# Kernel tuning notes

Measured on AMD Instinct MI355X. Metric: run time of the kernel, lower is better.

The kernel has to match this reference:

```python
import jax, jax.numpy as jnp
import numpy as np

RARITY_ALPHA = 0.5


def _forward(obs_emb, observed_mask, lengths, avg_interval, var_prior_emb_tensor,
             rarity_W, adjI, p2s_W1, p2s_b1, p2s_W2, p2s_b2,
             Wu, bu, Wr, br, Wc, bc):
    B, T, N, D = obs_emb.shape
    I = jnp.eye(N, dtype=obs_emb.dtype)
    # hypernetwork conditioning vector per node (prior_to_state MLP); identical
    # across batch since var_prior_emb_tensor is repeated over the batch dim.
    vv = jax.nn.relu(var_prior_emb_tensor @ p2s_W1 + p2s_b1) @ p2s_W2 + p2s_b2  # [N,E]
    vv = jnp.broadcast_to(vv[None], (B, N, vv.shape[-1]))                        # [B,N,E]
    tot = observed_mask.sum(axis=1)  # var_total_obs [B,N]

    def gate(z, W, b):
        # MLP_Param: per-node weights W_n = sum_e vv[n,e]*W[e]; fused einsum avoids
        # materializing [B,N,2D+1,D].
        return jnp.einsum('bni,bne,eio->bno', z, vv, W) + jnp.einsum('bne,eo->bno', vv, b)

    def step_fn(carry, xs):
        h, out = carry
        cur_obs, m, cur_avg, step = xs  # [B,N,D], [B,N], [B,N], scalar
        rs = RARITY_ALPHA * jnp.tanh(cur_avg / (tot + 1.0))                  # [B,N]
        rmat = -rarity_W * jnp.abs(rs[:, :, None] - rs[:, None, :])          # [B,N,N]
        # adj_mask[b,i,j] = observed(b,i)*observed(b,j)  (column-set then row-zero)
        adj_mask = m[:, :, None] * m[:, None, :]
        cur_adj = adjI * (1.0 + rmat) * adj_mask * (1.0 - I) + I             # [B,N,N]
        x = jnp.concatenate([cur_obs, rs[..., None]], axis=-1)              # [B,N,D+1]
        comb = jnp.einsum('bij,bjf->bif', cur_adj,
                          jnp.concatenate([x, h], axis=-1))                  # [B,N,2D+1]
        r = jax.nn.sigmoid(gate(comb, Wr, br))
        u = jax.nn.sigmoid(gate(comb, Wu, bu))
        mm = m[..., None] > 0
        h1 = jnp.where(mm, r * h, h)                      # h[nodes_ind] = r*h[nodes_ind]
        cand = jnp.tanh(gate(jnp.concatenate([x, h1], axis=-1), Wc, bc))
        h2 = jnp.where(mm, (1.0 - u) * h1 + u * cand, h1)  # scatter back at observed nodes
        out = jnp.where((step == lengths - 1)[:, None, None], h2, out)
        return (h2, out), None

    h0 = jnp.zeros((B, N, D), obs_emb.dtype)
    xs = (obs_emb.transpose(1, 0, 2, 3), observed_mask.transpose(1, 0, 2),
          avg_interval.transpose(1, 0, 2), jnp.arange(T))
    (_, out), _ = jax.lax.scan(step_fn, (h0, jnp.zeros_like(h0)), xs)
    return out


def setup_inputs() -> dict:
    B, T, N, D, E = 32, 64, 128, 64, 5
    key = jax.random.key(0)
    ks = jax.random.split(key, 18)
    inp = {}
    inp['obs_emb'] = jax.random.normal(ks[0], (B, T, N, D), jnp.float32)
    inp['adj'] = jax.random.normal(ks[1], (N, N), jnp.float32)  # unused by forward
    inp['observed_mask'] = (jax.random.uniform(ks[2], (B, T, N)) < 0.5).astype(jnp.float32)
    inp['observed_tp'] = jax.random.uniform(ks[3], (B, T), jnp.float32)       # unused
    inp['tp_emb_tensor'] = jax.random.normal(ks[4], (B, T, 1), jnp.float32)   # unused
    inp['lengths'] = jax.random.randint(ks[5], (B,), T // 2, T + 1, jnp.int32)
    inp['avg_interval'] = jax.random.uniform(ks[6], (B, T, N), jnp.float32)
    inp['var_prior_emb_tensor'] = jax.random.normal(ks[7], (N, 768), jnp.float32)
    # learned parameters
    inp['rarity_W'] = jax.random.normal(ks[8], (N, N), jnp.float32)
    inp['adjI'] = jnp.eye(N, dtype=jnp.float32) + 0.01 * jax.random.normal(ks[9], (N, N), jnp.float32)
    inp['p2s_W1'] = 0.05 * jax.random.normal(ks[10], (768, 2 * D), jnp.float32)
    inp['p2s_b1'] = jnp.zeros((2 * D,), jnp.float32)
    inp['p2s_W2'] = 0.1 * jax.random.normal(ks[11], (2 * D, E), jnp.float32)
    inp['p2s_b2'] = jnp.zeros((E,), jnp.float32)
    inp['Wu'] = 0.1 * jax.random.normal(ks[12], (E, 2 * D + 1, D), jnp.float32)
    inp['bu'] = 0.1 * jax.random.normal(ks[13], (E, D), jnp.float32)
    inp['Wr'] = 0.1 * jax.random.normal(ks[14], (E, 2 * D + 1, D), jnp.float32)
    inp['br'] = 0.1 * jax.random.normal(ks[15], (E, D), jnp.float32)
    inp['Wc'] = 0.1 * jax.random.normal(ks[16], (E, 2 * D + 1, D), jnp.float32)
    inp['bc'] = 0.1 * jax.random.normal(ks[17], (E, D), jnp.float32)
    return inp


def reference(obs_emb, adj, observed_mask, observed_tp, tp_emb_tensor, lengths,
              avg_interval, var_prior_emb_tensor, rarity_W, adjI, p2s_W1, p2s_b1,
              p2s_W2, p2s_b2, Wu, bu, Wr, br, Wc, bc):
    # adj, observed_tp, tp_emb_tensor are accepted but never used, as in the torch code
    return _forward(obs_emb, observed_mask, lengths, avg_interval, var_prior_emb_tensor,
                    rarity_W, adjI, p2s_W1, p2s_b1, p2s_W2, p2s_b2,
                    Wu, bu, Wr, br, Wc, bc)
```

## Files before the change

### kernel.cpp

```cpp
#include <hip/hip_runtime.h>
#include <math.h>

constexpr size_t WS_VV  = 1024;
constexpr size_t WS_TOT = 2048;
constexpr size_t WS_RS  = 8192;
constexpr size_t WS_WH  = 270336;
constexpr size_t WS_WX  = 1843200;
constexpr size_t WS_BF  = 3440640;
constexpr size_t WS_H   = 3465216;
constexpr size_t WS_CH  = 3727360;
constexpr size_t WS_CX  = 3989504;
constexpr size_t WS_GXR = 8249344;
constexpr size_t WS_GXU = 12443648;
constexpr size_t WS_CXC = 16637952;

__device__ __forceinline__ float sigm(float x){ return 1.f/(1.f+expf(-x)); }

__device__ __forceinline__ float2 ld2_mall(const float* p){
  union { unsigned long long u; float2 f; } cv;
  cv.u = __hip_atomic_load((const unsigned long long*)p, __ATOMIC_RELAXED,
                           __HIP_MEMORY_SCOPE_AGENT);
  return cv.f;
}
__device__ __forceinline__ void st2_mall(float* p, float a, float b){
  union { unsigned long long u; float2 f; } cv;
  cv.f = make_float2(a, b);
  __hip_atomic_store((unsigned long long*)p, cv.u, __ATOMIC_RELAXED,
                     __HIP_MEMORY_SCOPE_AGENT);
}

__global__ void k_vv(const float* __restrict__ vpe, const float* __restrict__ W1,
                     const float* __restrict__ b1, const float* __restrict__ W2,
                     const float* __restrict__ b2, float* __restrict__ ws){
  int n = blockIdx.x, tid = threadIdx.x;
  __shared__ float hid[128];
  if (tid < 128){
    float acc = b1[tid];
    for (int k=0;k<768;k++) acc = fmaf(vpe[n*768+k], W1[k*128+tid], acc);
    hid[tid] = fmaxf(acc, 0.f);
  }
  __syncthreads();
  if (tid < 5){
    float acc = b2[tid];
    for (int h=0;h<128;h++) acc = fmaf(hid[h], W2[h*5+tid], acc);
    ws[WS_VV + n*5 + tid] = acc;
  }
}

__global__ void k_fold(const float* __restrict__ Wr, const float* __restrict__ Wu,
                       const float* __restrict__ Wc, const float* __restrict__ br,
                       const float* __restrict__ bu, const float* __restrict__ bc,
                       float* __restrict__ ws){
  int bid = blockIdx.x; int g = bid>>7; int n = bid&127;
  const float* W  = (g==0)?Wr:(g==1)?Wu:Wc;
  const float* bb = (g==0)?br:(g==1)?bu:bc;
  float v[5];
#pragma unroll
  for (int e=0;e<5;e++) v[e] = ws[WS_VV + n*5 + e];
  for (int idx=threadIdx.x; idx<129*64; idx+=256){
    int i = idx>>6, o = idx&63;
    float a = 0.f;
#pragma unroll
    for (int e=0;e<5;e++) a = fmaf(v[e], W[(e*129+i)*64+o], a);
    if (i < 65) ws[WS_WX + (size_t)(g*128+n)*4160 + i*64 + o] = a;
    else        ws[WS_WH + (size_t)(g*128+n)*4096 + (i-65)*64 + o] = a;
  }
  if (threadIdx.x < 64){
    int o = threadIdx.x; float a = 0.f;
#pragma unroll
    for (int e=0;e<5;e++) a = fmaf(v[e], bb[e*64+o], a);
    ws[WS_BF + (g*128+n)*64 + o] = a;
  }
}

__global__ void k_tot(const float* __restrict__ mask, float* __restrict__ ws){
  int id = blockIdx.x*256 + threadIdx.x;
  int b = id>>7, n = id&127;
  float s = 0.f;
  for (int t=0;t<64;t++) s += mask[(b*64+t)*128 + n];
  ws[WS_TOT + b*128 + n] = s;
}

__global__ void k_rs(const float* __restrict__ avg, float* __restrict__ ws){
  int id = blockIdx.x*256 + threadIdx.x;
  int b = id>>13, n = id&127;
  float tot = ws[WS_TOT + b*128 + n];
  ws[WS_RS + id] = 0.5f * tanhf(avg[id] / (tot + 1.f));
}

__global__ __launch_bounds__(256) void p4a(const float* __restrict__ obs,
      const float* __restrict__ mask, const float* __restrict__ adjI,
      const float* __restrict__ rW, const int* __restrict__ lengths,
      float* __restrict__ ws, int c0){
  int rc = blockIdx.x;
  int b = rc>>4, tl = rc&15, t = c0 + tl;
  if (t >= lengths[b]) return;
  int rt = b*64 + t;
  __shared__ float xt[64*68];
  __shared__ float adjh[128*68];
  __shared__ float rs_l[128], m_l[128];
  int tid = threadIdx.x;
  if (tid < 128){ rs_l[tid] = ws[WS_RS + rt*128 + tid]; m_l[tid] = mask[rt*128 + tid]; }
  __syncthreads();
  int it = tid>>3, ft = tid&7, i0 = it*4, f0 = ft*8;
  float4 aL[4], aH[4]; float a64[4];
#pragma unroll
  for (int ii=0;ii<4;ii++){ aL[ii]=make_float4(0,0,0,0); aH[ii]=make_float4(0,0,0,0); a64[ii]=0.f; }
  for (int half=0; half<2; half++){
    __syncthreads();
    int j0 = half*64;
    for (int idx=tid; idx<4096; idx+=256){
      int jl = idx>>6, f = idx&63;
      xt[jl*68+f] = obs[(size_t)rt*8192 + (j0+jl)*64 + f];
    }
    if (tid < 64) xt[tid*68+64] = rs_l[j0+tid];
    for (int idx=tid; idx<8192; idx+=256){
      int i = idx>>6, jl = idx&63, j = j0+jl;
      float a;
      if (i == j) a = 1.f;
      else {
        int gi = i*128 + j;
        float dd = fabsf(rs_l[i] - rs_l[j]);
        a = adjI[gi] * (1.f - rW[gi]*dd) * m_l[i] * m_l[j];
      }
      adjh[i*68+jl] = a;
    }
    __syncthreads();
    for (int jb=0; jb<16; jb++){
      float4 av[4];
#pragma unroll
      for (int ii=0;ii<4;ii++) av[ii] = *(const float4*)&adjh[(i0+ii)*68 + jb*4];
#pragma unroll
      for (int jj=0;jj<4;jj++){
        int jl = jb*4 + jj;
        float4 xlo = *(const float4*)&xt[jl*68 + f0];
        float4 xhi = *(const float4*)&xt[jl*68 + f0 + 4];
        float xr = xt[jl*68 + 64];
#pragma unroll
        for (int ii=0;ii<4;ii++){
          float a = (jj==0)?av[ii].x:(jj==1)?av[ii].y:(jj==2)?av[ii].z:av[ii].w;
          aL[ii].x = fmaf(a, xlo.x, aL[ii].x); aL[ii].y = fmaf(a, xlo.y, aL[ii].y);
          aL[ii].z = fmaf(a, xlo.z, aL[ii].z); aL[ii].w = fmaf(a, xlo.w, aL[ii].w);
          aH[ii].x = fmaf(a, xhi.x, aH[ii].x); aH[ii].y = fmaf(a, xhi.y, aH[ii].y);
          aH[ii].z = fmaf(a, xhi.z, aH[ii].z); aH[ii].w = fmaf(a, xhi.w, aH[ii].w);
          a64[ii] = fmaf(a, xr, a64[ii]);
        }
      }
    }
  }
#pragma unroll
  for (int ii=0;ii<4;ii++){
    int i = i0 + ii;
    size_t base = WS_CX + (size_t)i*33280 + (size_t)rc*65 + f0;
    ws[base+0]=aL[ii].x; ws[base+1]=aL[ii].y; ws[base+2]=aL[ii].z; ws[base+3]=aL[ii].w;
    ws[base+4]=aH[ii].x; ws[base+5]=aH[ii].y; ws[base+6]=aH[ii].z; ws[base+7]=aH[ii].w;
    if (ft == 0) ws[WS_CX + (size_t)i*33280 + (size_t)rc*65 + 64] = a64[ii];
  }
}

__global__ __launch_bounds__(256) void p4b(const float* __restrict__ obs,
      const int* __restrict__ lengths, float* __restrict__ ws, int c0){
  int bid = blockIdx.x;
  int g = bid >> 9; int r2 = bid & 511; int n = r2 >> 2; int tile = r2 & 3;
  __shared__ float A[128*69];
  __shared__ float Wl[65*64];
  __shared__ float bl[64];
  __shared__ int slen[32];
  int tid = threadIdx.x;
  if (tid < 32) slen[tid] = lengths[tid];
  for (int idx=tid; idx<4160; idx+=256) Wl[idx] = ws[WS_WX + (size_t)(g*128+n)*4160 + idx];
  if (tid < 64) bl[tid] = ws[WS_BF + (g*128+n)*64 + tid];
  if (g < 2){
    const float* src = &ws[WS_CX + (size_t)n*33280 + (size_t)tile*8320];
    for (int idx=tid; idx<8320; idx+=256){
      int r = idx/65, f = idx - r*65;
      A[r*69+f] = src[idx];
    }
  } else {
    for (int idx=tid; idx<8320; idx+=256){
      int r = idx/65, f = idx - r*65;
      int grow = tile*128 + r;
      int gb = grow>>4, t = c0 + (grow&15);
      float v = (f < 64) ? obs[(size_t)(gb*64+t)*8192 + n*64 + f]
                         : ws[WS_RS + (gb*64+t)*128 + n];
      A[r*69+f] = v;
    }
  }
  __syncthreads();
  int rt8 = tid>>4, dq = tid&15;
  float4 acc[8];
#pragma unroll
  for (int rr=0;rr<8;rr++) acc[rr] = make_float4(0,0,0,0);
  for (int k=0;k<65;k++){
    float4 w = *(const float4*)&Wl[k*64 + dq*4];
#pragma unroll
    for (int rr=0;rr<8;rr++){
      float a = A[(rt8*8+rr)*69 + k];
      acc[rr].x = fmaf(a,w.x,acc[rr].x); acc[rr].y = fmaf(a,w.y,acc[rr].y);
      acc[rr].z = fmaf(a,w.z,acc[rr].z); acc[rr].w = fmaf(a,w.w,acc[rr].w);
    }
  }
  float4 b4 = *(const float4*)&bl[dq*4];
  float* dst = &ws[(g==0)?WS_GXR:(g==1)?WS_GXU:WS_CXC];
#pragma unroll
  for (int rr=0;rr<8;rr++){
    int grow = tile*128 + rt8*8 + rr;
    int gb = grow>>4, gtl = grow&15;
    if (c0 + gtl < slen[gb]){
      float4 o; o.x=acc[rr].x+b4.x; o.y=acc[rr].y+b4.y; o.z=acc[rr].z+b4.z; o.w=acc[rr].w+b4.w;
      *(float4*)&dst[((size_t)(n*16+gtl)*32 + gb)*64 + dq*4] = o;
    }
  }
}

__global__ __launch_bounds__(256) void krec(const float* __restrict__ mask,
      const int* __restrict__ lengths, const float* __restrict__ adjI,
      const float* __restrict__ rWm, float* __restrict__ out, float* __restrict__ ws,
      int c0){
  unsigned* hfl = (unsigned*)ws;
  const int bid = blockIdx.x, tid = threadIdx.x;
  const int bA = bid>>3, s = bid&7, ns = s*16;
  __shared__ float hs[8192];
  __shared__ float adjT[2560];
  __shared__ float chT[1088];
  __shared__ float hT[1088];
  __shared__ float rs_l[128], m_l[128];
  const int lenA = lengths[bA];
  const int ng = tid>>6, fA = tid&63;
  const int nl = tid>>4, fq = tid&15;
  const int n  = ns + nl;
  float* hbuf = &ws[WS_H];
  const float* wrg = &ws[WS_WH + (size_t)(0*128+n)*4096];
  const float* wug = &ws[WS_WH + (size_t)(1*128+n)*4096];
  const float* wcg = &ws[WS_WH + (size_t)(2*128+n)*4096];

  for (int t=c0; t<c0+16; t++){
    if (t >= lenA){
      if (tid == 0)
        __hip_atomic_store(&hfl[bid], (unsigned)(t+1), __ATOMIC_RELAXED,
                           __HIP_MEMORY_SCOPE_AGENT);
      __syncthreads();
      continue;
    }
    if (tid < 128) rs_l[tid] = ws[WS_RS + (size_t)(bA*64+t)*128 + tid];
    else           m_l[tid-128] = mask[(size_t)(bA*64+t)*128 + (tid-128)];
    __syncthreads();
    for (int idx=tid; idx<2048; idx+=256){
      int j = idx&127, il = idx>>7, I = ns+il;
      float a;
      if (I == j) a = 1.f;
      else {
        int gi = I*128 + j;
        float dd = fabsf(rs_l[I] - rs_l[j]);
        a = adjI[gi]*(1.f - rWm[gi]*dd)*m_l[I]*m_l[j];
      }
      adjT[j*20 + il] = a;
    }
    const int tl = t - c0;
    size_t gof = ((size_t)(n*16+tl)*32 + bA)*64 + fq*4;
    float4 arv = *(const float4*)&ws[WS_GXR + gof];
    float4 auv = *(const float4*)&ws[WS_GXU + gof];
    float4 acv = *(const float4*)&ws[WS_CXC + gof];
    float  msv = m_l[n];
    if (t > 0){
      if (tid < 8){
        unsigned tgt = (unsigned)t; int guard = 0;
        while (__hip_atomic_load(&hfl[bA*8 + tid], __ATOMIC_RELAXED,
                 __HIP_MEMORY_SCOPE_AGENT) < tgt && ++guard < (1<<20))
          __builtin_amdgcn_s_sleep(2);
      }
    }
    __syncthreads();
#pragma unroll
    for (int k=0;k<16;k++){
      int p = tid + 256*k;
      float2 v = ld2_mall(&hbuf[(size_t)bA*8192 + 2*p]);
      *(float2*)&hs[2*p] = v;
    }
    __syncthreads();
    float acc[4] = {0.f,0.f,0.f,0.f};
#pragma unroll 4
    for (int j=0;j<128;j++){
      float hv = hs[j*64 + fA];
      float4 a4 = *(const float4*)&adjT[j*20 + ng*4];
      acc[0] = fmaf(a4.x, hv, acc[0]);
      acc[1] = fmaf(a4.y, hv, acc[1]);
      acc[2] = fmaf(a4.z, hv, acc[2]);
      acc[3] = fmaf(a4.w, hv, acc[3]);
    }
#pragma unroll
    for (int r=0;r<4;r++) chT[(ng*4+r)*68 + fA] = acc[r];
    __syncthreads();
#pragma unroll 4
    for (int k=0;k<64;k++){
      float cv = chT[nl*68 + k];
      float4 wr4 = *(const float4*)&wrg[k*64 + fq*4];
      float4 wu4 = *(const float4*)&wug[k*64 + fq*4];
      arv.x = fmaf(cv,wr4.x,arv.x); arv.y = fmaf(cv,wr4.y,arv.y);
      arv.z = fmaf(cv,wr4.z,arv.z); arv.w = fmaf(cv,wr4.w,arv.w);
      auv.x = fmaf(cv,wu4.x,auv.x); auv.y = fmaf(cv,wu4.y,auv.y);
      auv.z = fmaf(cv,wu4.z,auv.z); auv.w = fmaf(cv,wu4.w,auv.w);
    }
    float4 rr4, uu4, h1;
    rr4.x = sigm(arv.x); rr4.y = sigm(arv.y); rr4.z = sigm(arv.z); rr4.w = sigm(arv.w);
    uu4.x = sigm(auv.x); uu4.y = sigm(auv.y); uu4.z = sigm(auv.z); uu4.w = sigm(auv.w);
    float4 hown = *(const float4*)&hs[n*64 + fq*4];
    bool ob = msv > 0.f;
    h1.x = ob ? rr4.x*hown.x : hown.x;
    h1.y = ob ? rr4.y*hown.y : hown.y;
    h1.z = ob ? rr4.z*hown.z : hown.z;
    h1.w = ob ? rr4.w*hown.w : hown.w;
    *(float4*)&hT[nl*68 + fq*4] = h1;
    __syncthreads();
#pragma unroll 4
    for (int k=0;k<64;k++){
      float hv1 = hT[nl*68 + k];
      float4 wc4 = *(const float4*)&wcg[k*64 + fq*4];
      acv.x = fmaf(hv1,wc4.x,acv.x); acv.y = fmaf(hv1,wc4.y,acv.y);
      acv.z = fmaf(hv1,wc4.z,acv.z); acv.w = fmaf(hv1,wc4.w,acv.w);
    }
    float4 cd, h2;
    cd.x = tanhf(acv.x); cd.y = tanhf(acv.y); cd.z = tanhf(acv.z); cd.w = tanhf(acv.w);
    h2.x = ob ? (1.f-uu4.x)*h1.x + uu4.x*cd.x : h1.x;
    h2.y = ob ? (1.f-uu4.y)*h1.y + uu4.y*cd.y : h1.y;
    h2.z = ob ? (1.f-uu4.z)*h1.z + uu4.z*cd.z : h1.z;
    h2.w = ob ? (1.f-uu4.w)*h1.w + uu4.w*cd.w : h1.w;
    float* hp = &hbuf[((size_t)bA*128 + n)*64 + fq*4];
    st2_mall(hp,   h2.x, h2.y);
    st2_mall(hp+2, h2.z, h2.w);
    if (t == lenA-1)
      *(float4*)&out[((size_t)bA*128 + n)*64 + fq*4] = h2;
    __syncthreads();
    asm volatile("s_waitcnt vmcnt(0)" ::: "memory");
    if (tid == 0)
      __hip_atomic_store(&hfl[bid], (unsigned)(t+1), __ATOMIC_RELAXED,
                         __HIP_MEMORY_SCOPE_AGENT);
  }
}

extern "C" void kernel_launch(void* const* d_in, const int* in_sizes, int n_in,
                              void* d_out, int out_size, void* d_ws, size_t ws_size,
                              hipStream_t stream){
  const float* obs  = (const float*)d_in[0];
  const float* maskp= (const float*)d_in[2];
  const int*   lens = (const int*)d_in[5];
  const float* avg  = (const float*)d_in[6];
  const float* vpe  = (const float*)d_in[7];
  const float* rW   = (const float*)d_in[8];
  const float* adjI = (const float*)d_in[9];
  const float* W1   = (const float*)d_in[10];
  const float* b1   = (const float*)d_in[11];
  const float* W2   = (const float*)d_in[12];
  const float* b2   = (const float*)d_in[13];
  const float* Wu   = (const float*)d_in[14];
  const float* bu   = (const float*)d_in[15];
  const float* Wr   = (const float*)d_in[16];
  const float* br   = (const float*)d_in[17];
  const float* Wc   = (const float*)d_in[18];
  const float* bc   = (const float*)d_in[19];
  float* out = (float*)d_out;
  float* ws  = (float*)d_ws;
  hipMemsetAsync(d_ws, 0, 4096, stream);
  hipMemsetAsync((char*)d_ws + WS_H*sizeof(float), 0, 262144*sizeof(float), stream);
  k_vv  <<<128, 256, 0, stream>>>(vpe, W1, b1, W2, b2, ws);
  k_fold<<<384, 256, 0, stream>>>(Wr, Wu, Wc, br, bu, bc, ws);
  k_tot <<<16,  256, 0, stream>>>(maskp, ws);
  k_rs  <<<1024,256, 0, stream>>>(avg, ws);
  for (int c = 0; c < 4; c++){
    int c0 = c*16;
    p4a <<<512, 256, 0, stream>>>(obs, maskp, adjI, rW, lens, ws, c0);
    p4b <<<1536,256, 0, stream>>>(obs, lens, ws, c0);
    krec<<<256, 256, 0, stream>>>(maskp, lens, adjI, rW, out, ws, c0);
  }
}
```

Before: 1.537 ms.

## Overlap recurrence with next-chunk projections in a fused double-buffered kernel

Time chunks shrink from 16 to 8 steps, and the adjacency-aggregation and input-projection workspaces become double-buffered. A single fused kernel per chunk runs the sequential recurrence blocks for chunk c alongside the aggregation (p4a) for chunk c+2 and the gate projections (p4b) for chunk c+1. Recurrence blocks get raised wave priority. The aim is to fill idle CUs during the latency-bound recurrence, which relies on cross-block spin-wait flags. The cost is twice as many launches and competition for memory bandwidth between the recurrence and the projection work.

```diff
diff --git a/kernel.cpp b/kernel.cpp
--- a/kernel.cpp
+++ b/kernel.cpp
@@ -8,11 +8,12 @@
 constexpr size_t WS_WX  = 1843200;
 constexpr size_t WS_BF  = 3440640;
 constexpr size_t WS_H   = 3465216;
-constexpr size_t WS_CH  = 3727360;
-constexpr size_t WS_CX  = 3989504;
-constexpr size_t WS_GXR = 8249344;
-constexpr size_t WS_GXU = 12443648;
-constexpr size_t WS_CXC = 16637952;
+constexpr size_t CXSZ   = 2129920;
+constexpr size_t GXSZ   = 2097152;
+constexpr size_t WS_CX0 = 3727360;
+constexpr size_t WS_GXR0= 7987200;
+constexpr size_t WS_GXU0= 12181504;
+constexpr size_t WS_CXC0= 16375808;
 
 __device__ __forceinline__ float sigm(float x){ return 1.f/(1.f+expf(-x)); }
 
@@ -88,17 +89,17 @@
   ws[WS_RS + id] = 0.5f * tanhf(avg[id] / (tot + 1.f));
 }
 
-__global__ __launch_bounds__(256) void p4a(const float* __restrict__ obs,
+__device__ void p4a_body(float* smem, const float* __restrict__ obs,
       const float* __restrict__ mask, const float* __restrict__ adjI,
       const float* __restrict__ rW, const int* __restrict__ lengths,
-      float* __restrict__ ws, int c0){
-  int rc = blockIdx.x;
-  int b = rc>>4, tl = rc&15, t = c0 + tl;
+      float* __restrict__ ws, int cc, int rc){
+  int b = rc>>3, tl = rc&7, t = cc*8 + tl;
   if (t >= lengths[b]) return;
   int rt = b*64 + t;
-  __shared__ float xt[64*68];
-  __shared__ float adjh[128*68];
-  __shared__ float rs_l[128], m_l[128];
+  float* xt   = smem;
+  float* adjh = smem + 4352;
+  float* rs_l = smem + 13056;
+  float* m_l  = smem + 13184;
   int tid = threadIdx.x;
   if (tid < 128){ rs_l[tid] = ws[WS_RS + rt*128 + tid]; m_l[tid] = mask[rt*128 + tid]; }
   __syncthreads();
@@ -148,30 +149,31 @@
       }
     }
   }
+  size_t cxb = WS_CX0 + (size_t)(cc&1)*CXSZ;
 #pragma unroll
   for (int ii=0;ii<4;ii++){
     int i = i0 + ii;
-    size_t base = WS_CX + (size_t)i*33280 + (size_t)rc*65 + f0;
+    size_t base = cxb + (size_t)i*16640 + (size_t)rc*65 + f0;
     ws[base+0]=aL[ii].x; ws[base+1]=aL[ii].y; ws[base+2]=aL[ii].z; ws[base+3]=aL[ii].w;
     ws[base+4]=aH[ii].x; ws[base+5]=aH[ii].y; ws[base+6]=aH[ii].z; ws[base+7]=aH[ii].w;
-    if (ft == 0) ws[WS_CX + (size_t)i*33280 + (size_t)rc*65 + 64] = a64[ii];
-  }
-}
-
-__global__ __launch_bounds__(256) void p4b(const float* __restrict__ obs,
-      const int* __restrict__ lengths, float* __restrict__ ws, int c0){
-  int bid = blockIdx.x;
-  int g = bid >> 9; int r2 = bid & 511; int n = r2 >> 2; int tile = r2 & 3;
-  __shared__ float A[128*69];
-  __shared__ float Wl[65*64];
-  __shared__ float bl[64];
-  __shared__ int slen[32];
+    if (ft == 0) ws[cxb + (size_t)i*16640 + (size_t)rc*65 + 64] = a64[ii];
+  }
+}
+
+__device__ void p4b_body(float* smem, const float* __restrict__ obs,
+      const int* __restrict__ lengths, float* __restrict__ ws, int cc, int pbid){
+  int g = pbid >> 8; int r2 = pbid & 255; int n = r2 >> 1; int tile = r2 & 1;
+  float* A  = smem;
+  float* Wl = smem + 8832;
+  float* bl = smem + 12992;
+  int* slen = (int*)(smem + 13056);
   int tid = threadIdx.x;
   if (tid < 32) slen[tid] = lengths[tid];
   for (int idx=tid; idx<4160; idx+=256) Wl[idx] = ws[WS_WX + (size_t)(g*128+n)*4160 + idx];
   if (tid < 64) bl[tid] = ws[WS_BF + (g*128+n)*64 + tid];
+  size_t cxb = WS_CX0 + (size_t)(cc&1)*CXSZ;
   if (g < 2){
-    const float* src = &ws[WS_CX + (size_t)n*33280 + (size_t)tile*8320];
+    const float* src = &ws[cxb + (size_t)n*16640 + (size_t)tile*8320];
     for (int idx=tid; idx<8320; idx+=256){
       int r = idx/65, f = idx - r*65;
       A[r*69+f] = src[idx];
@@ -180,7 +182,7 @@
     for (int idx=tid; idx<8320; idx+=256){
       int r = idx/65, f = idx - r*65;
       int grow = tile*128 + r;
-      int gb = grow>>4, t = c0 + (grow&15);
+      int gb = grow>>3, t = cc*8 + (grow&7);
       float v = (f < 64) ? obs[(size_t)(gb*64+t)*8192 + n*64 + f]
                          : ws[WS_RS + (gb*64+t)*128 + n];
       A[r*69+f] = v;
@@ -201,30 +203,32 @@
     }
   }
   float4 b4 = *(const float4*)&bl[dq*4];
-  float* dst = &ws[(g==0)?WS_GXR:(g==1)?WS_GXU:WS_CXC];
+  size_t gxb = ((g==0)?WS_GXR0:(g==1)?WS_GXU0:WS_CXC0) + (size_t)(cc&1)*GXSZ;
 #pragma unroll
   for (int rr=0;rr<8;rr++){
     int grow = tile*128 + rt8*8 + rr;
-    int gb = grow>>4, gtl = grow&15;
-    if (c0 + gtl < slen[gb]){
+    int gb = grow>>3, gtl = grow&7;
+    if (cc*8 + gtl < slen[gb]){
       float4 o; o.x=acc[rr].x+b4.x; o.y=acc[rr].y+b4.y; o.z=acc[rr].z+b4.z; o.w=acc[rr].w+b4.w;
-      *(float4*)&dst[((size_t)(n*16+gtl)*32 + gb)*64 + dq*4] = o;
-    }
-  }
-}
-
-__global__ __launch_bounds__(256) void krec(const float* __restrict__ mask,
+      *(float4*)&ws[gxb + ((size_t)(n*8+gtl)*32 + gb)*64 + dq*4] = o;
+    }
+  }
+}
+
+__device__ void krec_body(float* smem, const float* __restrict__ mask,
       const int* __restrict__ lengths, const float* __restrict__ adjI,
-      const float* __restrict__ rWm, float* __restrict__ out, float* __restrict__ ws,
-      int c0){
+      const float* __restrict__ rWm, float* __restrict__ out,
+      float* __restrict__ ws, int c){
+  __builtin_amdgcn_s_setprio(1);
   unsigned* hfl = (unsigned*)ws;
   const int bid = blockIdx.x, tid = threadIdx.x;
   const int bA = bid>>3, s = bid&7, ns = s*16;
-  __shared__ float hs[8192];
-  __shared__ float adjT[2560];
-  __shared__ float chT[1088];
-  __shared__ float hT[1088];
-  __shared__ float rs_l[128], m_l[128];
+  float* hs   = smem;
+  float* adjT = smem + 8192;
+  float* chT  = smem + 10752;
+  float* hT   = smem + 11840;
+  float* rs_l = smem + 12928;
+  float* m_l  = smem + 13056;
   const int lenA = lengths[bA];
   const int ng = tid>>6, fA = tid&63;
   const int nl = tid>>4, fq = tid&15;
@@ -233,8 +237,10 @@
   const float* wrg = &ws[WS_WH + (size_t)(0*128+n)*4096];
   const float* wug = &ws[WS_WH + (size_t)(1*128+n)*4096];
   const float* wcg = &ws[WS_WH + (size_t)(2*128+n)*4096];
-
-  for (int t=c0; t<c0+16; t++){
+  const int c0 = c*8;
+  const size_t gq = (size_t)(c&1)*GXSZ;
+
+  for (int t=c0; t<c0+8; t++){
     if (t >= lenA){
       if (tid == 0)
         __hip_atomic_store(&hfl[bid], (unsigned)(t+1), __ATOMIC_RELAXED,
@@ -257,10 +263,10 @@
       adjT[j*20 + il] = a;
     }
     const int tl = t - c0;
-    size_t gof = ((size_t)(n*16+tl)*32 + bA)*64 + fq*4;
-    float4 arv = *(const float4*)&ws[WS_GXR + gof];
-    float4 auv = *(const float4*)&ws[WS_GXU + gof];
-    float4 acv = *(const float4*)&ws[WS_CXC + gof];
+    size_t gof = ((size_t)(n*8+tl)*32 + bA)*64 + fq*4;
+    float4 arv = *(const float4*)&ws[WS_GXR0 + gq + gof];
+    float4 auv = *(const float4*)&ws[WS_GXU0 + gq + gof];
+    float4 acv = *(const float4*)&ws[WS_CXC0 + gq + gof];
     float  msv = m_l[n];
     if (t > 0){
       if (tid < 8){
@@ -336,6 +342,38 @@
       __hip_atomic_store(&hfl[bid], (unsigned)(t+1), __ATOMIC_RELAXED,
                          __HIP_MEMORY_SCOPE_AGENT);
   }
+}
+
+__global__ __launch_bounds__(256) void p4a_k(const float* __restrict__ obs,
+      const float* __restrict__ mask, const float* __restrict__ adjI,
+      const float* __restrict__ rW, const int* __restrict__ lengths,
+      float* __restrict__ ws, int cc){
+  __shared__ float smem[13312];
+  p4a_body(smem, obs, mask, adjI, rW, lengths, ws, cc, blockIdx.x);
+}
+__global__ __launch_bounds__(256) void p4b_k(const float* __restrict__ obs,
+      const int* __restrict__ lengths, float* __restrict__ ws, int cc){
+  __shared__ float smem[13312];
+  p4b_body(smem, obs, lengths, ws, cc, blockIdx.x);
+}
+
+__global__ __launch_bounds__(256) void kfused(const float* __restrict__ obs,
+      const float* __restrict__ mask, const float* __restrict__ adjI,
+      const float* __restrict__ rW, const int* __restrict__ lengths,
+      float* __restrict__ out, float* __restrict__ ws, int c){
+  __shared__ float smem[13312];
+  int bid = blockIdx.x;
+  if (bid < 256){
+    krec_body(smem, mask, lengths, adjI, rW, out, ws, c);
+    return;
+  }
+  bool has4a = (c < 6);
+  if (has4a && bid < 512){
+    p4a_body(smem, obs, mask, adjI, rW, lengths, ws, c+2, bid-256);
+    return;
+  }
+  int pb = bid - (has4a ? 512 : 256);
+  p4b_body(smem, obs, lengths, ws, c+1, pb);
 }
 
 extern "C" void kernel_launch(void* const* d_in, const int* in_sizes, int n_in,
@@ -366,10 +404,11 @@
   k_fold<<<384, 256, 0, stream>>>(Wr, Wu, Wc, br, bu, bc, ws);
   k_tot <<<16,  256, 0, stream>>>(maskp, ws);
   k_rs  <<<1024,256, 0, stream>>>(avg, ws);
-  for (int c = 0; c < 4; c++){
-    int c0 = c*16;
-    p4a <<<512, 256, 0, stream>>>(obs, maskp, adjI, rW, lens, ws, c0);
-    p4b <<<1536,256, 0, stream>>>(obs, lens, ws, c0);
-    krec<<<256, 256, 0, stream>>>(maskp, lens, adjI, rW, out, ws, c0);
-  }
-}
+  p4a_k<<<256, 256, 0, stream>>>(obs, maskp, adjI, rW, lens, ws, 0);
+  p4a_k<<<256, 256, 0, stream>>>(obs, maskp, adjI, rW, lens, ws, 1);
+  p4b_k<<<768, 256, 0, stream>>>(obs, lens, ws, 0);
+  for (int c = 0; c < 8; c++){
+    int grid = (c <= 5) ? 1280 : (c == 6) ? 1024 : 256;
+    kfused<<<grid, 256, 0, stream>>>(obs, maskp, adjI, rW, lens, out, ws, c);
+  }
+}
```

Measured after the change: 1.432 ms. 1.07x faster.
